# Kernel optimization log

Hardware: AMD Instinct MI355X
Metric: run time of the kernel (lower is better)

Reference implementation:

```python
import jax, jax.numpy as jnp
import numpy as np

S_STA = 32          # s_sta_dim
N_TS = 4            # n_timesteps
NUM_FREQ = 4        # NeRF PE octaves -> 2 + 2*2*4 = 18 PE channels
EPS_NORM = 1e-12    # torch F.normalize default eps


def pos_enc_concat(v):
    # v: (B, C, H, W) -> concat NeRF positional encoding of pixel grid on channel dim
    B, C, H, W = v.shape
    ys = jnp.linspace(-1.0, 1.0, H)
    xs = jnp.linspace(-1.0, 1.0, W)
    coords = jnp.stack(jnp.meshgrid(ys, xs, indexing='ij'), axis=0)  # (2, H, W)
    feats = [coords]
    for i in range(NUM_FREQ):
        f = (2.0 ** i) * jnp.pi * coords
        feats.append(jnp.sin(f))
        feats.append(jnp.cos(f))
    pe = jnp.concatenate(feats, axis=0).astype(v.dtype)              # (18, H, W)
    pe = jnp.broadcast_to(pe[None], (B,) + pe.shape)
    return jnp.concatenate([v, pe], axis=1)


def setup_inputs() -> dict:
    key = jax.random.key(0)
    k1, k2, k3 = jax.random.split(key, 3)
    ch = 128
    x = jax.random.normal(k1, (4, 4, 12, ch, 24, 24), dtype=jnp.float32)
    Wv = jax.random.normal(k2, (ch, ch), dtype=jnp.float32) / np.float32(np.sqrt(ch))
    bv = jax.random.normal(k3, (ch,), dtype=jnp.float32) * 0.01
    return {"x": x, "Wv": Wv, "bv": bv, "temp": 1}


def reference(x, Wv, bv, temp):
    bs, N, T, ch, h, w = x.shape
    BN, hw = bs * N, h * w
    scale = ch ** (-0.5)
    xf = x.reshape(BN, T, ch, h, w)

    # F.normalize(p=2, dim=-3): L2-normalize over channel dim
    nrm = jnp.sqrt(jnp.sum(xf * xf, axis=2, keepdims=True))
    x_att = xf / jnp.maximum(nrm, EPS_NORM)

    qs = x_att[:, 1:].reshape(BN * (T - 1), ch, hw)
    ks = x_att[:, :-1].reshape(BN * (T - 1), ch, hw)
    energy = jnp.einsum('bcn,bcm->bnm', qs, ks).reshape(BN, T - 1, hw, hw) * scale
    attn = jax.nn.softmax(energy / temp, axis=-1)       # (BN, T-1, hw, hw)

    # to_v: 1x1 conv then NeRF PE concat
    v = jnp.einsum('oc,btchw->btohw', Wv, xf) + bv[None, None, :, None, None]
    v = pos_enc_concat(v.reshape(BN * T, ch, h, w))     # (BN*T, ch+18, h, w)
    vs_pe = v.reshape(BN, T, -1, hw)                    # (BN, T, C_v, hw)

    Tp = T - N_TS + 1
    acc = vs_pe[:, :Tp, S_STA:]                         # (BN, Tp, C_v-S_STA, hw)
    for t in range(N_TS - 1):                           # small fixed recurrence depth
        cs = vs_pe[:, t + 1:t + 1 + Tp, S_STA:]
        ca = attn[:, t:t + Tp]
        prop = jnp.einsum('btcm,btnm->btcn', acc, ca)
        acc = jnp.concatenate([cs, prop], axis=2)
    return acc
```

## Files before the change

### kernel.cpp

```cpp
#include <hip/hip_runtime.h>
#include <math.h>

#define BN 16
#define T 12
#define CH 128
#define HW 576
#define TM1 11
#define TP 9
#define CCS 114

typedef __attribute__((ext_vector_type(8))) short bf16x8;
typedef __attribute__((ext_vector_type(4))) float floatx4;

__device__ inline float b2f(unsigned short u) {
    unsigned int v = ((unsigned int)u) << 16;
    return __builtin_bit_cast(float, v);
}
__device__ inline unsigned short f2b(float f) {
    unsigned int v = __builtin_bit_cast(unsigned int, f);
    unsigned int r = (v + 0x7FFFu + ((v >> 16) & 1u)) >> 16;
    return (unsigned short)r;
}

__device__ __forceinline__ void async_copy16(void* lds, const void* g) {
    __builtin_amdgcn_global_load_lds(
        (const __attribute__((address_space(1))) unsigned int*)g,
        (__attribute__((address_space(3))) unsigned int*)lds,
        16, 0, 0);
}

__global__ __launch_bounds__(256) void k_norm_t(const float* __restrict__ x,
                                                unsigned short* __restrict__ xT) {
    int bt = blockIdx.x / 9;
    int p0 = (blockIdx.x % 9) * 64;
    int t = threadIdx.x;
    int lane = t & 63, wave = t >> 6;
    int pq = t & 15;
    int cg = t >> 4;
    const float* src = x + (size_t)bt * CH * HW + (size_t)(cg * 8) * HW + p0 + pq * 4;

    floatx4 v[8];
    float s0 = 0.f, s1 = 0.f, s2 = 0.f, s3 = 0.f;
#pragma unroll
    for (int j = 0; j < 8; j++) {
        v[j] = *(const floatx4*)(src + (size_t)j * HW);
        s0 = fmaf(v[j][0], v[j][0], s0);
        s1 = fmaf(v[j][1], v[j][1], s1);
        s2 = fmaf(v[j][2], v[j][2], s2);
        s3 = fmaf(v[j][3], v[j][3], s3);
    }
#pragma unroll
    for (int m = 16; m < 64; m <<= 1) {
        s0 += __shfl_xor(s0, m);
        s1 += __shfl_xor(s1, m);
        s2 += __shfl_xor(s2, m);
        s3 += __shfl_xor(s3, m);
    }
    __shared__ float smP[4][16][4];
    __shared__ float smI[64];
    if (lane < 16) {
        smP[wave][lane][0] = s0; smP[wave][lane][1] = s1;
        smP[wave][lane][2] = s2; smP[wave][lane][3] = s3;
    }
    __syncthreads();
    if (t < 64) {
        int q = t >> 2, k = t & 3;
        float tot = smP[0][q][k] + smP[1][q][k] + smP[2][q][k] + smP[3][q][k];
        smI[t] = 1.0f / fmaxf(sqrtf(tot), 1e-12f);
    }
    __syncthreads();
    unsigned short* dst = xT + ((size_t)bt * HW + p0 + pq * 4) * CH + cg * 8;
#pragma unroll
    for (int k = 0; k < 4; k++) {
        float inv = smI[pq * 4 + k];
        union { unsigned short u[8]; uint4 q4; } pk;
#pragma unroll
        for (int j = 0; j < 8; j++) pk.u[j] = f2b(v[j][k] * inv);
        *(uint4*)(dst + (size_t)k * CH) = pk.q4;
    }
}

__global__ __launch_bounds__(256, 2) void k_energysm(const unsigned short* __restrict__ xT,
                                                     unsigned short* __restrict__ attn,
                                                     const int* __restrict__ temp) {
    int nwg = gridDim.x;
    int wg = (blockIdx.x & 7) * (nwg >> 3) + (blockIdx.x >> 3);
    int z = wg / 18, nt = wg % 18;
    int b = z / TM1, ti = z % TM1;
    const unsigned short* Q = xT + (size_t)(b * T + ti + 1) * HW * CH;
    const unsigned short* K = xT + (size_t)(b * T + ti) * HW * CH;
    unsigned short* A = attn + (size_t)z * HW * HW;
    int n0 = nt * 32;

    int lane = threadIdx.x & 63, wave = threadIdx.x >> 6;
    int fr = lane & 15, hi = lane >> 4;
    int m0 = wave * 144;

    __shared__ char smB[2 * 36864];
    __shared__ float smMax[4][32];
    __shared__ float smSum[4][32];

    bf16x8 af[4][2];
#pragma unroll
    for (int k0 = 0; k0 < 4; k0++)
#pragma unroll
        for (int fi = 0; fi < 2; fi++)
            af[k0][fi] = *(const bf16x8*)(Q + (size_t)(n0 + fi * 16 + fr) * CH + k0 * 32 + hi * 8);

    int tt = threadIdx.x;
    int rw = tt >> 2;
    int scp = (tt & 3) ^ ((rw >> 1) & 3);
    const unsigned short* srcB[9];
#pragma unroll
    for (int g = 0; g < 9; g++)
        srcB[g] = K + (size_t)(g * 64 + rw) * CH + scp * 8;

    int xc = (fr >> 1) & 3;
    int boff[9];
#pragma unroll
    for (int j = 0; j < 9; j++)
        boff[j] = (m0 + j * 16 + fr) * 64 + ((hi ^ xc) << 4);

#pragma unroll
    for (int g = 0; g < 9; g++)
        async_copy16(smB + g * 4096 + wave * 1024, srcB[g]);
    __syncthreads();

    floatx4 acc[2][9] = {};
#pragma unroll
    for (int s = 0; s < 4; s++) {
        if (s < 3) {
            char* nb = smB + ((s + 1) & 1) * 36864 + wave * 1024;
#pragma unroll
            for (int g = 0; g < 9; g++)
                async_copy16(nb + g * 4096, srcB[g] + (s + 1) * 32);
        }
        const char* cb = smB + (s & 1) * 36864;
        bf16x8 bfr[9];
#pragma unroll
        for (int j = 0; j < 9; j++) bfr[j] = *(const bf16x8*)(cb + boff[j]);
#pragma unroll
        for (int fi = 0; fi < 2; fi++)
#pragma unroll
            for (int j = 0; j < 9; j++)
                acc[fi][j] = __builtin_amdgcn_mfma_f32_16x16x32_bf16(af[s][fi], bfr[j], acc[fi][j], 0, 0, 0);
        __syncthreads();
    }

    float sc = 0.08838834764831845f / (float)temp[0];

    float pm[2][4];
#pragma unroll
    for (int fi = 0; fi < 2; fi++)
#pragma unroll
        for (int reg = 0; reg < 4; reg++) {
            float m = acc[fi][0][reg];
#pragma unroll
            for (int j = 1; j < 9; j++) m = fmaxf(m, acc[fi][j][reg]);
#pragma unroll
            for (int msk = 1; msk < 16; msk <<= 1) m = fmaxf(m, __shfl_xor(m, msk));
            pm[fi][reg] = m;
        }
    if (fr == 0) {
#pragma unroll
        for (int fi = 0; fi < 2; fi++)
#pragma unroll
            for (int reg = 0; reg < 4; reg++)
                smMax[wave][fi * 16 + hi * 4 + reg] = pm[fi][reg];
    }
    __syncthreads();

    float rmax[2][4];
#pragma unroll
    for (int fi = 0; fi < 2; fi++)
#pragma unroll
        for (int reg = 0; reg < 4; reg++) {
            int row = fi * 16 + hi * 4 + reg;
            rmax[fi][reg] = fmaxf(fmaxf(smMax[0][row], smMax[1][row]),
                                  fmaxf(smMax[2][row], smMax[3][row]));
        }

    float ps[2][4];
#pragma unroll
    for (int fi = 0; fi < 2; fi++)
#pragma unroll
        for (int reg = 0; reg < 4; reg++) {
            float s = 0.f;
#pragma unroll
            for (int j = 0; j < 9; j++) {
                float e = __expf(sc * (acc[fi][j][reg] - rmax[fi][reg]));
                acc[fi][j][reg] = e;
                s += e;
            }
#pragma unroll
            for (int msk = 1; msk < 16; msk <<= 1) s += __shfl_xor(s, msk);
            ps[fi][reg] = s;
        }
    if (fr == 0) {
#pragma unroll
        for (int fi = 0; fi < 2; fi++)
#pragma unroll
            for (int reg = 0; reg < 4; reg++)
                smSum[wave][fi * 16 + hi * 4 + reg] = ps[fi][reg];
    }
    __syncthreads();

#pragma unroll
    for (int fi = 0; fi < 2; fi++)
#pragma unroll
        for (int reg = 0; reg < 4; reg++) {
            int row = fi * 16 + hi * 4 + reg;
            float inv = 1.0f / (smSum[0][row] + smSum[1][row] + smSum[2][row] + smSum[3][row]);
            int n = n0 + row;
#pragma unroll
            for (int j = 0; j < 9; j++)
                A[(size_t)n * HW + m0 + j * 16 + fr] = f2b(acc[fi][j][reg] * inv);
        }
}

__global__ __launch_bounds__(256) void k_vgemm(const float* __restrict__ x,
                                               const float* __restrict__ Wv,
                                               const float* __restrict__ bv,
                                               unsigned short* __restrict__ cs16,
                                               float* __restrict__ out) {
    int bt = blockIdx.z;
    int b = bt / T, t = bt % T;
    const float* X = x + (size_t)bt * CH * HW;
    unsigned short* C16 = cs16 + (size_t)bt * CCS * HW;
    float* O = (t >= 3) ? out + (size_t)(b * TP + t - 3) * 456 * HW : nullptr;
    int m0 = blockIdx.y * 64, n0 = blockIdx.x * 64;
    __shared__ float As[16][66];
    __shared__ float Bs[16][66];
    int tid = threadIdx.x;
    int kq = tid % 16, lr = tid / 16;
    int tx = tid % 16, ty = tid / 16;
    int lp = tid % 64, lc = tid / 64;
    float acc[4][4] = {};
    for (int c0 = 0; c0 < CH; c0 += 16) {
#pragma unroll
        for (int i = 0; i < 4; i++) {
            int r = m0 + lr + 16 * i;
            As[kq][lr + 16 * i] = (r < 96) ? Wv[(size_t)(32 + r) * CH + c0 + kq] : 0.f;
        }
#pragma unroll
        for (int i = 0; i < 4; i++) {
            int c = lc + 4 * i;
            Bs[c][lp] = X[(size_t)(c0 + c) * HW + n0 + lp];
        }
        __syncthreads();
#pragma unroll
        for (int kk = 0; kk < 16; kk++) {
            float2 a01 = *(const float2*)&As[kk][ty * 4];
            float2 a23 = *(const float2*)&As[kk][ty * 4 + 2];
            float2 b01 = *(const float2*)&Bs[kk][tx * 4];
            float2 b23 = *(const float2*)&Bs[kk][tx * 4 + 2];
            float av[4] = {a01.x, a01.y, a23.x, a23.y};
            float bw[4] = {b01.x, b01.y, b23.x, b23.y};
#pragma unroll
            for (int i = 0; i < 4; i++)
#pragma unroll
                for (int j = 0; j < 4; j++)
                    acc[i][j] = fmaf(av[i], bw[j], acc[i][j]);
        }
        __syncthreads();
    }
#pragma unroll
    for (int i = 0; i < 4; i++) {
        int r = m0 + ty * 4 + i;
        if (r < 96) {
            float bb = bv[32 + r];
            floatx4 o;
            o[0] = acc[i][0] + bb; o[1] = acc[i][1] + bb;
            o[2] = acc[i][2] + bb; o[3] = acc[i][3] + bb;
            union { unsigned short u[4]; uint2 v; } pk;
            pk.u[0] = f2b(o[0]); pk.u[1] = f2b(o[1]); pk.u[2] = f2b(o[2]); pk.u[3] = f2b(o[3]);
            *(uint2*)(C16 + (size_t)r * HW + n0 + tx * 4) = pk.v;
            if (O) __builtin_nontemporal_store(o, (floatx4*)(O + (size_t)r * HW + n0 + tx * 4));
        }
    }
}

__global__ __launch_bounds__(576) void k_pe(unsigned short* __restrict__ cs16,
                                            float* __restrict__ out) {
    int bt = blockIdx.x;
    int b = bt / T, t = bt % T;
    int p = threadIdx.x;
    unsigned short* C16 = cs16 + ((size_t)bt * CCS + 96) * HW + p;
    float* O = (t >= 3) ? out + ((size_t)(b * TP + t - 3) * 456 + 96) * HW + p : nullptr;
    int iy = p / 24, ix = p % 24;
    float y = -1.f + 2.f * (float)iy / 23.f;
    float xx = -1.f + 2.f * (float)ix / 23.f;
    float vals[18];
    vals[0] = y; vals[1] = xx;
    const float PI = 3.14159265358979323846f;
#pragma unroll
    for (int i = 0; i < 4; i++) {
        float k = (float)(1 << i) * PI;
        float fy = k * y, fx = k * xx;
        vals[2 + 4 * i + 0] = sinf(fy);
        vals[2 + 4 * i + 1] = sinf(fx);
        vals[2 + 4 * i + 2] = cosf(fy);
        vals[2 + 4 * i + 3] = cosf(fx);
    }
#pragma unroll
    for (int c = 0; c < 18; c++) {
        C16[(size_t)c * HW] = f2b(vals[c]);
        if (O) __builtin_nontemporal_store(vals[c], O + (size_t)c * HW);
    }
}

template<int M_, bool F32OUT>
__global__ __launch_bounds__(256) void k_stage(const unsigned short* __restrict__ cs16,
                                               const unsigned short* __restrict__ prop_in,
                                               const unsigned short* __restrict__ attn,
                                               float* __restrict__ dst_f32,
                                               unsigned short* __restrict__ dst_b16,
                                               int tshift, int prop_ch,
                                               int dst_stride_ch, int dst_ch_off) {
    constexpr int MT = (M_ + 127) / 128;
    constexpr int WPZ = MT * 6;
    constexpr int BUFSZ = 28672;

    int nwg = gridDim.x;
    int wg = (blockIdx.x & 7) * (nwg >> 3) + (blockIdx.x >> 3);
    int z = wg / WPZ;
    int rem = wg % WPZ;
    int mt = rem / 6, nt = rem % 6;
    int m0 = mt * 128, n0 = nt * 96;

    int b = z / TP, tp = z % TP;
    const unsigned short* csz = cs16 + (size_t)((b * T + tp + tshift) * CCS) * HW;
    const unsigned short* prz = prop_in ? prop_in + (size_t)z * prop_ch * HW : csz;
    const unsigned short* Bm = attn + (size_t)(b * TM1 + tp + tshift) * HW * HW;

    __shared__ uint4 smq[2 * BUFSZ / 16];
    char* smc = (char*)smq;

    int tid = threadIdx.x;
    int lane = tid & 63, wave = tid >> 6;
    int wm = wave >> 1, wn = wave & 1;
    int fr = lane & 15, hi = lane >> 4;

    int cp = tid & 7;
    int rloc = tid >> 3;
    const unsigned short* srcA[4];
#pragma unroll
    for (int i = 0; i < 4; i++) {
        int r = i * 32 + rloc;
        int rg = m0 + r;
        const unsigned short* p;
        if (rg < CCS) p = csz + (size_t)rg * HW;
        else if (rg < M_) p = prz + (size_t)(rg - CCS) * HW;
        else p = csz;
        srcA[i] = p + ((cp ^ (r & 7)) << 3);
    }
    const unsigned short* srcB[3];
#pragma unroll
    for (int i = 0; i < 3; i++) {
        int r = i * 32 + rloc;
        srcB[i] = Bm + (size_t)(n0 + r) * HW + ((cp ^ (r & 7)) << 3);
    }

    int arow[4], brow[3];
#pragma unroll
    for (int i = 0; i < 4; i++) arow[i] = (wm * 64 + i * 16 + fr) * 128;
#pragma unroll
    for (int j = 0; j < 3; j++) brow[j] = (wn * 48 + j * 16 + fr) * 128;
    int xr = fr & 7;

    floatx4 acc[4][3] = {};
    int buf = 0;

    {
        char* base = smc;
        int wo = wave * 1024;
#pragma unroll
        for (int i = 0; i < 4; i++) async_copy16(base + i * 4096 + wo, srcA[i]);
#pragma unroll
        for (int i = 0; i < 3; i++) async_copy16(base + 16384 + i * 4096 + wo, srcB[i]);
    }
    __syncthreads();

    for (int t = 0; t < 9; ++t) {
        if (t < 8) {
            char* nb = smc + (buf ^ 1) * BUFSZ;
            int wo = wave * 1024;
            int ko = (t + 1) * 64;
#pragma unroll
            for (int i = 0; i < 4; i++) async_copy16(nb + i * 4096 + wo, srcA[i] + ko);
#pragma unroll
            for (int i = 0; i < 3; i++) async_copy16(nb + 16384 + i * 4096 + wo, srcB[i] + ko);
        }
        char* base = smc + buf * BUFSZ;
#pragma unroll
        for (int s = 0; s < 2; ++s) {
            int coff = ((s * 4 + hi) ^ xr) << 4;
            bf16x8 af[4], bfr[3];
#pragma unroll
            for (int i = 0; i < 4; i++) af[i] = *(const bf16x8*)(base + arow[i] + coff);
#pragma unroll
            for (int j = 0; j < 3; j++) bfr[j] = *(const bf16x8*)(base + 16384 + brow[j] + coff);
#pragma unroll
            for (int i = 0; i < 4; i++)
#pragma unroll
                for (int j = 0; j < 3; j++)
                    acc[i][j] = __builtin_amdgcn_mfma_f32_16x16x32_bf16(af[i], bfr[j], acc[i][j], 0, 0, 0);
        }
        __syncthreads();
        buf ^= 1;
    }

    int crow = hi * 4, ccol = fr;
#pragma unroll
    for (int i = 0; i < 4; i++) {
#pragma unroll
        for (int reg = 0; reg < 4; reg++) {
            int r = m0 + wm * 64 + i * 16 + crow + reg;
            if (r < M_) {
#pragma unroll
                for (int j = 0; j < 3; j++) {
                    int n = n0 + wn * 48 + j * 16 + ccol;
                    size_t idx = ((size_t)z * dst_stride_ch + dst_ch_off + r) * HW + n;
                    if (F32OUT) __builtin_nontemporal_store(acc[i][j][reg], dst_f32 + idx);
                    else dst_b16[idx] = f2b(acc[i][j][reg]);
                }
            }
        }
    }
}

extern "C" void kernel_launch(void* const* d_in, const int* in_sizes, int n_in,
                              void* d_out, int out_size, void* d_ws, size_t ws_size,
                              hipStream_t stream) {
    const float* x  = (const float*)d_in[0];
    const float* Wv = (const float*)d_in[1];
    const float* bv = (const float*)d_in[2];
    const int* temp = (const int*)d_in[3];
    float* out = (float*)d_out;

    char* w = (char*)d_ws;
    unsigned short* xT     = (unsigned short*)w;
    w += (size_t)192 * HW * CH * 2;
    unsigned short* attn16 = (unsigned short*)w;
    w += (size_t)176 * HW * HW * 2;
    unsigned short* cs16   = (unsigned short*)w;
    w += (size_t)192 * CCS * HW * 2;
    unsigned short* p1     = (unsigned short*)w;
    w += (size_t)144 * CCS * HW * 2;
    unsigned short* p2     = (unsigned short*)w;

    k_norm_t<<<192 * 9, 256, 0, stream>>>(x, xT);
    k_energysm<<<dim3(3168), 256, 0, stream>>>(xT, attn16, temp);
    k_vgemm<<<dim3(9, 2, 192), 256, 0, stream>>>(x, Wv, bv, cs16, out);
    k_pe<<<192, 576, 0, stream>>>(cs16, out);
    k_stage<114, false><<<dim3(864),  256, 0, stream>>>(cs16, nullptr, attn16, nullptr, p1, 0, 0, 114, 0);
    k_stage<228, false><<<dim3(1728), 256, 0, stream>>>(cs16, p1, attn16, nullptr, p2, 1, 114, 228, 0);
    k_stage<342, true ><<<dim3(2592), 256, 0, stream>>>(cs16, p2, attn16, out, nullptr, 2, 228, 456, 114);
}
```

Measured before the change: 479.4 us.

## Fuse first propagation stage into energy-softmax kernel using LDS-resident attention tile

The energy/softmax kernel now also writes its normalized attention tile into shared memory and, for the timesteps that feed the first propagation stage, multiplies the 114-channel value slice by that tile to produce p1 directly. The separate first k_stage launch and its re-read of attention from global memory are removed. To make this legal, the vgemm and positional-encoding kernels are reordered ahead of the energy kernel so cs16 is ready. The trade-off is extra work and LDS traffic inside an already heavy kernel, plus a strided unpadded-reuse of smB that may cause bank conflicts.

```diff
diff --git a/kernel.cpp b/kernel.cpp
--- a/kernel.cpp
+++ b/kernel.cpp
@@ -82,6 +82,8 @@
 
 __global__ __launch_bounds__(256, 2) void k_energysm(const unsigned short* __restrict__ xT,
                                                      unsigned short* __restrict__ attn,
+                                                     const unsigned short* __restrict__ cs16,
+                                                     unsigned short* __restrict__ p1,
                                                      const int* __restrict__ temp) {
     int nwg = gridDim.x;
     int wg = (blockIdx.x & 7) * (nwg >> 3) + (blockIdx.x >> 3);
@@ -205,6 +207,7 @@
     }
     __syncthreads();
 
+    constexpr int PP = 584;
 #pragma unroll
     for (int fi = 0; fi < 2; fi++)
 #pragma unroll
@@ -213,8 +216,52 @@
             float inv = 1.0f / (smSum[0][row] + smSum[1][row] + smSum[2][row] + smSum[3][row]);
             int n = n0 + row;
 #pragma unroll
-            for (int j = 0; j < 9; j++)
-                A[(size_t)n * HW + m0 + j * 16 + fr] = f2b(acc[fi][j][reg] * inv);
+            for (int j = 0; j < 9; j++) {
+                int m = m0 + j * 16 + fr;
+                unsigned short pv = f2b(acc[fi][j][reg] * inv);
+                A[(size_t)n * HW + m] = pv;
+                *(unsigned short*)(smB + (size_t)row * (PP * 2) + m * 2) = pv;
+            }
+        }
+
+    if (ti > 8) return;
+    __syncthreads();
+
+    const unsigned short* csz = cs16 + (size_t)((b * T + ti) * CCS) * HW;
+    unsigned short* p1z = p1 + (size_t)(b * TP + ti) * CCS * HW;
+    int rbase = wave * 32;
+
+    floatx4 acc2[2][2] = {};
+#pragma unroll
+    for (int ks = 0; ks < 18; ks++) {
+        bf16x8 afr[2], pfr[2];
+#pragma unroll
+        for (int rf = 0; rf < 2; rf++) {
+            int r = rbase + rf * 16 + fr;
+            int rr = (r < CCS) ? r : 0;
+            afr[rf] = *(const bf16x8*)(csz + (size_t)rr * HW + ks * 32 + hi * 8);
+        }
+#pragma unroll
+        for (int nf = 0; nf < 2; nf++)
+            pfr[nf] = *(const bf16x8*)(smB + (size_t)(nf * 16 + fr) * (PP * 2) + ks * 64 + hi * 16);
+#pragma unroll
+        for (int rf = 0; rf < 2; rf++)
+#pragma unroll
+            for (int nf = 0; nf < 2; nf++)
+                acc2[rf][nf] = __builtin_amdgcn_mfma_f32_16x16x32_bf16(afr[rf], pfr[nf], acc2[rf][nf], 0, 0, 0);
+    }
+#pragma unroll
+    for (int rf = 0; rf < 2; rf++)
+#pragma unroll
+        for (int reg = 0; reg < 4; reg++) {
+            int r = rbase + rf * 16 + hi * 4 + reg;
+            if (r < CCS) {
+#pragma unroll
+                for (int nf = 0; nf < 2; nf++) {
+                    int n = n0 + nf * 16 + fr;
+                    p1z[(size_t)r * HW + n] = f2b(acc2[rf][nf][reg]);
+                }
+            }
         }
 }
 
@@ -450,10 +497,9 @@
     unsigned short* p2     = (unsigned short*)w;
 
     k_norm_t<<<192 * 9, 256, 0, stream>>>(x, xT);
-    k_energysm<<<dim3(3168), 256, 0, stream>>>(xT, attn16, temp);
     k_vgemm<<<dim3(9, 2, 192), 256, 0, stream>>>(x, Wv, bv, cs16, out);
     k_pe<<<192, 576, 0, stream>>>(cs16, out);
-    k_stage<114, false><<<dim3(864),  256, 0, stream>>>(cs16, nullptr, attn16, nullptr, p1, 0, 0, 114, 0);
+    k_energysm<<<dim3(3168), 256, 0, stream>>>(xT, attn16, cs16, p1, temp);
     k_stage<228, false><<<dim3(1728), 256, 0, stream>>>(cs16, p1, attn16, nullptr, p2, 1, 114, 228, 0);
     k_stage<342, true ><<<dim3(2592), 256, 0, stream>>>(cs16, p2, attn16, out, nullptr, 2, 228, 456, 114);
 }
```

New measurement: 472.5 us (median of 2 runs). No clear change (-1.4%).
